# Optimization experiments

Hardware: AMD Instinct MI355X
Metric: run time of the kernel (lower is better)

Reference implementation:

```python
import jax, jax.numpy as jnp
import numpy as np

B, N, K = 4, 8192, 32
HID, INP = 64, 64
IN_CH = HID + INP  # 128; SetConv fc1 sees IN_CH + 3 (relative pos)


def setup_inputs() -> dict:
    key = jax.random.key(0)
    ks = jax.random.split(key, 10)
    return {
        "h": jax.random.normal(ks[0], (B, N, HID), jnp.float32),
        "x": jax.random.normal(ks[1], (B, N, INP), jnp.float32),
        "c": jax.random.normal(ks[2], (B, N, 3), jnp.float32),
        "W1": jax.random.normal(ks[3], (3, IN_CH + 3, HID), jnp.float32) * 0.05,
        "b1": jnp.zeros((3, HID), jnp.float32),
        "W2": jax.random.normal(ks[4], (3, HID, HID), jnp.float32) * 0.05,
        "b2": jnp.zeros((3, HID), jnp.float32),
        "W3": jax.random.normal(ks[5], (3, HID, HID), jnp.float32) * 0.05,
        "b3": jnp.zeros((3, HID), jnp.float32),
        "neigh_idx": jax.random.randint(ks[6], (B, N, K), 0, N, jnp.int32),
        "edge_feats": jax.random.normal(ks[7], (B, N, K, 3), jnp.float32),
    }


def reference(h, x, c, W1, b1, W2, b2, W3, b3, neigh_idx, edge_feats):
    # c (point coordinates) is unused by the GRU body, matching the torch source.
    slope = 0.1

    def setconv(i, feat):
        # gather K neighbor features per point: [B, N, K, C]
        g = jax.vmap(lambda fb, ib: fb[ib])(feat, neigh_idx)
        e = jnp.concatenate([g, edge_feats], axis=-1)  # [B, N, K, C+3]
        y = jax.nn.leaky_relu(jnp.einsum('bnkc,cd->bnkd', e, W1[i]) + b1[i], slope)
        y = y.max(axis=2)  # pool over neighbors -> [B, N, HID]
        y = jax.nn.leaky_relu(y @ W2[i] + b2[i], slope)
        return y @ W3[i] + b3[i]

    hx = jnp.concatenate([h, x], axis=2)
    z = jax.nn.sigmoid(setconv(0, hx))
    r = jax.nn.sigmoid(setconv(1, hx))
    q = jnp.tanh(setconv(2, jnp.concatenate([r * h, x], axis=2)))
    return (1.0 - z) * h + z * q
```

## Files before the change

### kernel.cpp

```cpp
#include <hip/hip_runtime.h>
#include <math.h>

typedef unsigned short u16;
typedef unsigned int u32;

#define KNBR 32

__device__ __forceinline__ float bf2f(u16 u) { return __uint_as_float((u32)u << 16); }
__device__ __forceinline__ float bflo(u32 u) { return __uint_as_float(u << 16); }
__device__ __forceinline__ float bfhi(u32 u) { return __uint_as_float(u & 0xffff0000u); }
__device__ __forceinline__ u16 f2bf(float f) {
    u32 u = __float_as_uint(f);
    return (u16)((u + 0x7fffu + ((u >> 16) & 1u)) >> 16);
}
__device__ __forceinline__ u32 pk2(float a, float b) {
    return (u32)f2bf(a) | ((u32)f2bf(b) << 16);
}
__device__ __forceinline__ float leaky(float v) { return v >= 0.f ? v : 0.1f * v; }
__device__ __forceinline__ float sigm(float v) { return 1.f / (1.f + expf(-v)); }

__device__ __forceinline__ int swz_plb(int b, int full) {
    if (!full) return b << 6;
    int xcd = b & 7;
    int within = ((b >> 3) << 1) | (xcd & 1);
    return ((xcd >> 1) << 13) + (within << 6);
}


__global__ __launch_bounds__(512) void k_gemm_p01(
    const float* __restrict__ h, const float* __restrict__ x,
    const float* __restrict__ W1f, const float* __restrict__ b1f,
    u32* __restrict__ P01, int p0, int full)
{
    __shared__ u32 a_lds[64 * 65];
    __shared__ float w_lds[2][64 * 64];
    int t = threadIdx.x;
    int plb = swz_plb(blockIdx.x, full);
    int pgb = p0 + plb;
    for (int i = 0; i < 8; ++i) {
        int id = t + i * 512;
        int p = id >> 6, cw = id & 63;
        const float* src = (cw < 32) ? (h + (size_t)(pgb + p) * 64 + cw * 2)
                                     : (x + (size_t)(pgb + p) * 64 + (cw - 32) * 2);
        float2 v = *(const float2*)src;
        a_lds[p * 65 + cw] = pk2(v.x, v.y);
    }
    int lane = t & 63;
    int cg = __builtin_amdgcn_readfirstlane(t >> 6);
    int di = lane & 15, pi = lane >> 4;
    int pt0 = cg * 8 + pi * 2;
    int dch = di * 4;
    float acc0[2][4], acc1[2][4];
    float4 bv0 = *(const float4*)&b1f[dch];
    float4 bv1 = *(const float4*)&b1f[64 + dch];
    #pragma unroll
    for (int pp = 0; pp < 2; ++pp) {
        acc0[pp][0] = bv0.x; acc0[pp][1] = bv0.y; acc0[pp][2] = bv0.z; acc0[pp][3] = bv0.w;
        acc1[pp][0] = bv1.x; acc1[pp][1] = bv1.y; acc1[pp][2] = bv1.z; acc1[pp][3] = bv1.w;
    }
    for (int half = 0; half < 2; ++half) {
        __syncthreads();
        for (int i = 0; i < 4; ++i) {
            int id = t + i * 512;
            int g = id >> 10, r = (id >> 4) & 63, d4 = id & 15;
            *(float4*)&w_lds[g][r * 64 + d4 * 4] =
                *(const float4*)(W1f + g * 8384 + (half * 64 + r) * 64 + d4 * 4);
        }
        __syncthreads();
        #pragma unroll 4
        for (int cw = 0; cw < 32; ++cw) {
            u32 aw0 = a_lds[(pt0 + 0) * 65 + half * 32 + cw];
            u32 aw1 = a_lds[(pt0 + 1) * 65 + half * 32 + cw];
            float4 wa0 = *(float4*)&w_lds[0][(2 * cw) * 64 + dch];
            float4 wa1 = *(float4*)&w_lds[0][(2 * cw + 1) * 64 + dch];
            float4 wb0 = *(float4*)&w_lds[1][(2 * cw) * 64 + dch];
            float4 wb1 = *(float4*)&w_lds[1][(2 * cw + 1) * 64 + dch];
            float a00 = bflo(aw0), a01 = bfhi(aw0);
            float a10 = bflo(aw1), a11 = bfhi(aw1);
            acc0[0][0] = fmaf(a00, wa0.x, acc0[0][0]); acc0[0][1] = fmaf(a00, wa0.y, acc0[0][1]);
            acc0[0][2] = fmaf(a00, wa0.z, acc0[0][2]); acc0[0][3] = fmaf(a00, wa0.w, acc0[0][3]);
            acc0[0][0] = fmaf(a01, wa1.x, acc0[0][0]); acc0[0][1] = fmaf(a01, wa1.y, acc0[0][1]);
            acc0[0][2] = fmaf(a01, wa1.z, acc0[0][2]); acc0[0][3] = fmaf(a01, wa1.w, acc0[0][3]);
            acc0[1][0] = fmaf(a10, wa0.x, acc0[1][0]); acc0[1][1] = fmaf(a10, wa0.y, acc0[1][1]);
            acc0[1][2] = fmaf(a10, wa0.z, acc0[1][2]); acc0[1][3] = fmaf(a10, wa0.w, acc0[1][3]);
            acc0[1][0] = fmaf(a11, wa1.x, acc0[1][0]); acc0[1][1] = fmaf(a11, wa1.y, acc0[1][1]);
            acc0[1][2] = fmaf(a11, wa1.z, acc0[1][2]); acc0[1][3] = fmaf(a11, wa1.w, acc0[1][3]);
            acc1[0][0] = fmaf(a00, wb0.x, acc1[0][0]); acc1[0][1] = fmaf(a00, wb0.y, acc1[0][1]);
            acc1[0][2] = fmaf(a00, wb0.z, acc1[0][2]); acc1[0][3] = fmaf(a00, wb0.w, acc1[0][3]);
            acc1[0][0] = fmaf(a01, wb1.x, acc1[0][0]); acc1[0][1] = fmaf(a01, wb1.y, acc1[0][1]);
            acc1[0][2] = fmaf(a01, wb1.z, acc1[0][2]); acc1[0][3] = fmaf(a01, wb1.w, acc1[0][3]);
            acc1[1][0] = fmaf(a10, wb0.x, acc1[1][0]); acc1[1][1] = fmaf(a10, wb0.y, acc1[1][1]);
            acc1[1][2] = fmaf(a10, wb0.z, acc1[1][2]); acc1[1][3] = fmaf(a10, wb0.w, acc1[1][3]);
            acc1[1][0] = fmaf(a11, wb1.x, acc1[1][0]); acc1[1][1] = fmaf(a11, wb1.y, acc1[1][1]);
            acc1[1][2] = fmaf(a11, wb1.z, acc1[1][2]); acc1[1][3] = fmaf(a11, wb1.w, acc1[1][3]);
        }
    }
    #pragma unroll
    for (int pp = 0; pp < 2; ++pp) {
        u32 o[4];
        #pragma unroll
        for (int j = 0; j < 4; ++j) o[j] = pk2(acc0[pp][j], acc1[pp][j]);
        *(uint4*)(P01 + (size_t)(plb + pt0 + pp) * 64 + dch) = *(uint4*)o;
    }
}

__global__ __launch_bounds__(512) void k_fuse01(
    const u32* __restrict__ P01, const float* __restrict__ W1f,
    const int* __restrict__ nidx, const float* __restrict__ ef,
    const float* __restrict__ h, const float* __restrict__ x,
    const float* __restrict__ W2f, const float* __restrict__ b2f,
    const float* __restrict__ W3f, const float* __restrict__ b3f,
    const float* __restrict__ b1f,
    u16* __restrict__ Z, u16* __restrict__ P2, int p0, int full)
{
    __shared__ u32 a_lds[64 * 65];
    __shared__ float w_lds[2][64 * 64];
    int t = threadIdx.x;
    int plb = swz_plb(blockIdx.x, full);
    int lane = t & 63;
    int cg = __builtin_amdgcn_readfirstlane(t >> 6);

    for (int i = 0; i < 4; ++i) {
        int id = t + i * 512;
        int g = id >> 10, r = (id >> 4) & 63, d4 = id & 15;
        *(float4*)&w_lds[g][r * 64 + d4 * 4] =
            *(const float4*)(W2f + g * 4096 + r * 64 + d4 * 4);
    }
    {
        u16* y16 = (u16*)a_lds;
        float w00 = W1f[8192 + lane], w01 = W1f[8256 + lane], w02 = W1f[8320 + lane];
        float w10 = W1f[16576 + lane], w11 = W1f[16640 + lane], w12 = W1f[16704 + lane];
        for (int pp = 0; pp < 8; ++pp) {
            int lp = cg * 8 + pp;
            int pg = p0 + plb + lp;
            int rbase = ((pg >> 13) << 13) - p0;
            const int* ni = nidx + (size_t)pg * KNBR;
            const float* ep = ef + (size_t)pg * KNBR * 3;
            float m0 = -1e30f, m1 = -1e30f;
            #pragma unroll 16
            for (int k = 0; k < KNBR; ++k) {
                int lr = rbase + ni[k];
                u32 g = P01[(size_t)lr * 64 + lane];
                float e0 = ep[3 * k], e1 = ep[3 * k + 1], e2 = ep[3 * k + 2];
                m0 = fmaxf(m0, bflo(g) + e0 * w00 + e1 * w01 + e2 * w02);
                m1 = fmaxf(m1, bfhi(g) + e0 * w10 + e1 * w11 + e2 * w12);
            }
            y16[lp * 130 + lane]      = f2bf(leaky(m0));
            y16[lp * 130 + 64 + lane] = f2bf(leaky(m1));
        }
    }
    __syncthreads();
    int g = cg >> 2, q = cg & 3;
    int di = lane & 15, pi = lane >> 4;
    int pt0 = q * 16 + pi * 4;
    int dch = di * 4;
    float acc[4][4];
    {
        float4 bv = *(const float4*)&b2f[g * 64 + dch];
        #pragma unroll
        for (int pp = 0; pp < 4; ++pp) {
            acc[pp][0] = bv.x; acc[pp][1] = bv.y; acc[pp][2] = bv.z; acc[pp][3] = bv.w;
        }
    }
    #pragma unroll 2
    for (int cw = 0; cw < 32; ++cw) {
        u32 aw[4];
        #pragma unroll
        for (int pp = 0; pp < 4; ++pp) aw[pp] = a_lds[(pt0 + pp) * 65 + g * 32 + cw];
        float4 w0 = *(float4*)&w_lds[g][(2 * cw) * 64 + dch];
        float4 w1 = *(float4*)&w_lds[g][(2 * cw + 1) * 64 + dch];
        #pragma unroll
        for (int pp = 0; pp < 4; ++pp) {
            float a0 = bflo(aw[pp]), a1 = bfhi(aw[pp]);
            acc[pp][0] = fmaf(a0, w0.x, acc[pp][0]);
            acc[pp][1] = fmaf(a0, w0.y, acc[pp][1]);
            acc[pp][2] = fmaf(a0, w0.z, acc[pp][2]);
            acc[pp][3] = fmaf(a0, w0.w, acc[pp][3]);
            acc[pp][0] = fmaf(a1, w1.x, acc[pp][0]);
            acc[pp][1] = fmaf(a1, w1.y, acc[pp][1]);
            acc[pp][2] = fmaf(a1, w1.z, acc[pp][2]);
            acc[pp][3] = fmaf(a1, w1.w, acc[pp][3]);
        }
    }
    __syncthreads();
    #pragma unroll
    for (int pp = 0; pp < 4; ++pp) {
        int base = (pt0 + pp) * 65 + g * 32 + di * 2;
        a_lds[base]     = pk2(leaky(acc[pp][0]), leaky(acc[pp][1]));
        a_lds[base + 1] = pk2(leaky(acc[pp][2]), leaky(acc[pp][3]));
    }
    for (int i = 0; i < 4; ++i) {
        int id = t + i * 512;
        int gg = id >> 10, r = (id >> 4) & 63, d4 = id & 15;
        *(float4*)&w_lds[gg][r * 64 + d4 * 4] =
            *(const float4*)(W3f + gg * 4096 + r * 64 + d4 * 4);
    }
    __syncthreads();
    {
        float4 bv = *(const float4*)&b3f[g * 64 + dch];
        #pragma unroll
        for (int pp = 0; pp < 4; ++pp) {
            acc[pp][0] = bv.x; acc[pp][1] = bv.y; acc[pp][2] = bv.z; acc[pp][3] = bv.w;
        }
    }
    #pragma unroll 2
    for (int cw = 0; cw < 32; ++cw) {
        u32 aw[4];
        #pragma unroll
        for (int pp = 0; pp < 4; ++pp) aw[pp] = a_lds[(pt0 + pp) * 65 + g * 32 + cw];
        float4 w0 = *(float4*)&w_lds[g][(2 * cw) * 64 + dch];
        float4 w1 = *(float4*)&w_lds[g][(2 * cw + 1) * 64 + dch];
        #pragma unroll
        for (int pp = 0; pp < 4; ++pp) {
            float a0 = bflo(aw[pp]), a1 = bfhi(aw[pp]);
            acc[pp][0] = fmaf(a0, w0.x, acc[pp][0]);
            acc[pp][1] = fmaf(a0, w0.y, acc[pp][1]);
            acc[pp][2] = fmaf(a0, w0.z, acc[pp][2]);
            acc[pp][3] = fmaf(a0, w0.w, acc[pp][3]);
            acc[pp][0] = fmaf(a1, w1.x, acc[pp][0]);
            acc[pp][1] = fmaf(a1, w1.y, acc[pp][1]);
            acc[pp][2] = fmaf(a1, w1.z, acc[pp][2]);
            acc[pp][3] = fmaf(a1, w1.w, acc[pp][3]);
        }
    }
    __syncthreads();
    if (g == 0) {
        #pragma unroll
        for (int pp = 0; pp < 4; ++pp) {
            int pl = plb + pt0 + pp;
            uint2 o;
            o.x = pk2(sigm(acc[pp][0]), sigm(acc[pp][1]));
            o.y = pk2(sigm(acc[pp][2]), sigm(acc[pp][3]));
            *(uint2*)(Z + (size_t)pl * 64 + dch) = o;
        }
    } else {
        #pragma unroll
        for (int pp = 0; pp < 4; ++pp) {
            int pg = p0 + plb + pt0 + pp;
            float4 hv = *(const float4*)&h[(size_t)pg * 64 + dch];
            int base = (pt0 + pp) * 65 + di * 2;
            a_lds[base]     = pk2(sigm(acc[pp][0]) * hv.x, sigm(acc[pp][1]) * hv.y);
            a_lds[base + 1] = pk2(sigm(acc[pp][2]) * hv.z, sigm(acc[pp][3]) * hv.w);
        }
    }
    for (int i = 0; i < 4; ++i) {
        int id = t + i * 512;
        int p = id >> 5, cw = id & 31;
        float2 v = *(const float2*)(x + (size_t)(p0 + plb + p) * 64 + cw * 2);
        a_lds[p * 65 + 32 + cw] = pk2(v.x, v.y);
    }
    float* wflat = (float*)w_lds;
    for (int i = 0; i < 4; ++i) {
        int id = t + i * 512;
        int r = id >> 4, d4 = id & 15;
        *(float4*)&wflat[r * 64 + d4 * 4] =
            *(const float4*)(W1f + 2 * 8384 + r * 64 + d4 * 4);
    }
    __syncthreads();
    int pt0b = cg * 8 + pi * 2;
    float pacc[2][4];
    {
        float4 bv = *(const float4*)&b1f[128 + dch];
        #pragma unroll
        for (int pp = 0; pp < 2; ++pp) {
            pacc[pp][0] = bv.x; pacc[pp][1] = bv.y; pacc[pp][2] = bv.z; pacc[pp][3] = bv.w;
        }
    }
    #pragma unroll 2
    for (int cw = 0; cw < 64; ++cw) {
        u32 aw0 = a_lds[(pt0b + 0) * 65 + cw];
        u32 aw1 = a_lds[(pt0b + 1) * 65 + cw];
        float4 w0 = *(float4*)&wflat[(2 * cw) * 64 + dch];
        float4 w1 = *(float4*)&wflat[(2 * cw + 1) * 64 + dch];
        float a00 = bflo(aw0), a01 = bfhi(aw0);
        float a10 = bflo(aw1), a11 = bfhi(aw1);
        pacc[0][0] = fmaf(a00, w0.x, pacc[0][0]); pacc[0][1] = fmaf(a00, w0.y, pacc[0][1]);
        pacc[0][2] = fmaf(a00, w0.z, pacc[0][2]); pacc[0][3] = fmaf(a00, w0.w, pacc[0][3]);
        pacc[0][0] = fmaf(a01, w1.x, pacc[0][0]); pacc[0][1] = fmaf(a01, w1.y, pacc[0][1]);
        pacc[0][2] = fmaf(a01, w1.z, pacc[0][2]); pacc[0][3] = fmaf(a01, w1.w, pacc[0][3]);
        pacc[1][0] = fmaf(a10, w0.x, pacc[1][0]); pacc[1][1] = fmaf(a10, w0.y, pacc[1][1]);
        pacc[1][2] = fmaf(a10, w0.z, pacc[1][2]); pacc[1][3] = fmaf(a10, w0.w, pacc[1][3]);
        pacc[1][0] = fmaf(a11, w1.x, pacc[1][0]); pacc[1][1] = fmaf(a11, w1.y, pacc[1][1]);
        pacc[1][2] = fmaf(a11, w1.z, pacc[1][2]); pacc[1][3] = fmaf(a11, w1.w, pacc[1][3]);
    }
    #pragma unroll
    for (int pp = 0; pp < 2; ++pp) {
        int pl = plb + pt0b + pp;
        uint2 o;
        o.x = pk2(pacc[pp][0], pacc[pp][1]);
        o.y = pk2(pacc[pp][2], pacc[pp][3]);
        *(uint2*)(P2 + (size_t)pl * 64 + dch) = o;
    }
}

__global__ __launch_bounds__(512) void k_fuse2(
    const u16* __restrict__ P2, const float* __restrict__ W1f,
    const int* __restrict__ nidx, const float* __restrict__ ef,
    const float* __restrict__ W2f, const float* __restrict__ b2f,
    const float* __restrict__ W3f, const float* __restrict__ b3f,
    const float* __restrict__ h, const u16* __restrict__ Z,
    float* __restrict__ out, int p0, int full)
{
    __shared__ u32 a_lds[64 * 33];
    __shared__ float w_lds[64 * 64];
    int t = threadIdx.x;
    int plb = swz_plb(blockIdx.x, full);
    int lane = t & 63;
    int cg = __builtin_amdgcn_readfirstlane(t >> 6);
    for (int i = 0; i < 2; ++i) {
        int id = t + i * 512;
        int r = (id >> 4) & 63, d4 = id & 15;
        *(float4*)&w_lds[r * 64 + d4 * 4] =
            *(const float4*)(W2f + 2 * 4096 + r * 64 + d4 * 4);
    }
    {
        const float* W = W1f + 2 * 8384;
        float w0 = W[8192 + lane], w1 = W[8256 + lane], w2 = W[8320 + lane];
        u16* y16 = (u16*)a_lds;
        for (int pp = 0; pp < 8; ++pp) {
            int lp = cg * 8 + pp;
            int pg = p0 + plb + lp;
            int rbase = ((pg >> 13) << 13) - p0;
            const int* ni = nidx + (size_t)pg * KNBR;
            const float* ep = ef + (size_t)pg * KNBR * 3;
            float m = -1e30f;
            #pragma unroll 16
            for (int k = 0; k < KNBR; ++k) {
                int lr = rbase + ni[k];
                float e0 = ep[3 * k], e1 = ep[3 * k + 1], e2 = ep[3 * k + 2];
                float v = bf2f(P2[(size_t)lr * 64 + lane]) + e0 * w0 + e1 * w1 + e2 * w2;
                m = fmaxf(m, v);
            }
            y16[lp * 66 + lane] = f2bf(leaky(m));
        }
    }
    __syncthreads();
    int di = lane & 15, pi = lane >> 4;
    int pt0 = cg * 8 + pi * 2;
    int dch = di * 4;
    float acc[2][4];
    {
        float4 bv = *(const float4*)&b2f[128 + dch];
        #pragma unroll
        for (int pp = 0; pp < 2; ++pp) {
            acc[pp][0] = bv.x; acc[pp][1] = bv.y; acc[pp][2] = bv.z; acc[pp][3] = bv.w;
        }
    }
    #pragma unroll 2
    for (int cw = 0; cw < 32; ++cw) {
        u32 aw0 = a_lds[(pt0 + 0) * 33 + cw];
        u32 aw1 = a_lds[(pt0 + 1) * 33 + cw];
        float4 w0 = *(float4*)&w_lds[(2 * cw) * 64 + dch];
        float4 w1 = *(float4*)&w_lds[(2 * cw + 1) * 64 + dch];
        float a00 = bflo(aw0), a01 = bfhi(aw0);
        float a10 = bflo(aw1), a11 = bfhi(aw1);
        acc[0][0] = fmaf(a00, w0.x, acc[0][0]); acc[0][1] = fmaf(a00, w0.y, acc[0][1]);
        acc[0][2] = fmaf(a00, w0.z, acc[0][2]); acc[0][3] = fmaf(a00, w0.w, acc[0][3]);
        acc[0][0] = fmaf(a01, w1.x, acc[0][0]); acc[0][1] = fmaf(a01, w1.y, acc[0][1]);
        acc[0][2] = fmaf(a01, w1.z, acc[0][2]); acc[0][3] = fmaf(a01, w1.w, acc[0][3]);
        acc[1][0] = fmaf(a10, w0.x, acc[1][0]); acc[1][1] = fmaf(a10, w0.y, acc[1][1]);
        acc[1][2] = fmaf(a10, w0.z, acc[1][2]); acc[1][3] = fmaf(a10, w0.w, acc[1][3]);
        acc[1][0] = fmaf(a11, w1.x, acc[1][0]); acc[1][1] = fmaf(a11, w1.y, acc[1][1]);
        acc[1][2] = fmaf(a11, w1.z, acc[1][2]); acc[1][3] = fmaf(a11, w1.w, acc[1][3]);
    }
    __syncthreads();
    #pragma unroll
    for (int pp = 0; pp < 2; ++pp) {
        int base = (pt0 + pp) * 33 + di * 2;
        a_lds[base]     = pk2(leaky(acc[pp][0]), leaky(acc[pp][1]));
        a_lds[base + 1] = pk2(leaky(acc[pp][2]), leaky(acc[pp][3]));
    }
    for (int i = 0; i < 2; ++i) {
        int id = t + i * 512;
        int r = (id >> 4) & 63, d4 = id & 15;
        *(float4*)&w_lds[r * 64 + d4 * 4] =
            *(const float4*)(W3f + 2 * 4096 + r * 64 + d4 * 4);
    }
    __syncthreads();
    {
        float4 bv = *(const float4*)&b3f[128 + dch];
        #pragma unroll
        for (int pp = 0; pp < 2; ++pp) {
            acc[pp][0] = bv.x; acc[pp][1] = bv.y; acc[pp][2] = bv.z; acc[pp][3] = bv.w;
        }
    }
    #pragma unroll 2
    for (int cw = 0; cw < 32; ++cw) {
        u32 aw0 = a_lds[(pt0 + 0) * 33 + cw];
        u32 aw1 = a_lds[(pt0 + 1) * 33 + cw];
        float4 w0 = *(float4*)&w_lds[(2 * cw) * 64 + dch];
        float4 w1 = *(float4*)&w_lds[(2 * cw + 1) * 64 + dch];
        float a00 = bflo(aw0), a01 = bfhi(aw0);
        float a10 = bflo(aw1), a11 = bfhi(aw1);
        acc[0][0] = fmaf(a00, w0.x, acc[0][0]); acc[0][1] = fmaf(a00, w0.y, acc[0][1]);
        acc[0][2] = fmaf(a00, w0.z, acc[0][2]); acc[0][3] = fmaf(a00, w0.w, acc[0][3]);
        acc[0][0] = fmaf(a01, w1.x, acc[0][0]); acc[0][1] = fmaf(a01, w1.y, acc[0][1]);
        acc[0][2] = fmaf(a01, w1.z, acc[0][2]); acc[0][3] = fmaf(a01, w1.w, acc[0][3]);
        acc[1][0] = fmaf(a10, w0.x, acc[1][0]); acc[1][1] = fmaf(a10, w0.y, acc[1][1]);
        acc[1][2] = fmaf(a10, w0.z, acc[1][2]); acc[1][3] = fmaf(a10, w0.w, acc[1][3]);
        acc[1][0] = fmaf(a11, w1.x, acc[1][0]); acc[1][1] = fmaf(a11, w1.y, acc[1][1]);
        acc[1][2] = fmaf(a11, w1.z, acc[1][2]); acc[1][3] = fmaf(a11, w1.w, acc[1][3]);
    }
    #pragma unroll
    for (int pp = 0; pp < 2; ++pp) {
        int pl = plb + pt0 + pp;
        int pg = p0 + pl;
        float4 hv = *(const float4*)&h[(size_t)pg * 64 + dch];
        uint2 zw = *(const uint2*)(Z + (size_t)pl * 64 + dch);
        float z0 = bflo(zw.x), z1 = bfhi(zw.x), z2 = bflo(zw.y), z3 = bfhi(zw.y);
        float4 o;
        o.x = (1.f - z0) * hv.x + z0 * tanhf(acc[pp][0]);
        o.y = (1.f - z1) * hv.y + z1 * tanhf(acc[pp][1]);
        o.z = (1.f - z2) * hv.z + z2 * tanhf(acc[pp][2]);
        o.w = (1.f - z3) * hv.w + z3 * tanhf(acc[pp][3]);
        *(float4*)&out[(size_t)pg * 64 + dch] = o;
    }
}

extern "C" void kernel_launch(void* const* d_in, const int* in_sizes, int n_in,
                              void* d_out, int out_size, void* d_ws, size_t ws_size,
                              hipStream_t stream)
{
    const float* h  = (const float*)d_in[0];
    const float* x  = (const float*)d_in[1];
    const float* W1 = (const float*)d_in[3];
    const float* b1 = (const float*)d_in[4];
    const float* W2 = (const float*)d_in[5];
    const float* b2 = (const float*)d_in[6];
    const float* W3 = (const float*)d_in[7];
    const float* b3 = (const float*)d_in[8];
    const int* nidx = (const int*)d_in[9];
    const float* ef = (const float*)d_in[10];
    float* out = (float*)d_out;

    char* wsb = (char*)d_ws;
    size_t PN = (ws_size >= 32768ull * 512ull) ? 32768 : 8192;
    int passes = (int)(32768 / PN);
    int full = (PN == 32768) ? 1 : 0;

    u32* P01 = (u32*)wsb;
    u16* Z   = (u16*)(wsb + PN * 256);
    u16* P2  = (u16*)(wsb + PN * 384);

    for (int s = 0; s < passes; ++s) {
        int p0 = (int)(s * PN);
        dim3 g((unsigned)(PN / 64));
        k_gemm_p01<<<g, 512, 0, stream>>>(h, x, W1, b1, P01, p0, full);
        k_fuse01  <<<g, 512, 0, stream>>>(P01, W1, nidx, ef, h, x,
                                          W2, b2, W3, b3, b1, Z, P2, p0, full);
        k_fuse2   <<<g, 512, 0, stream>>>(P2, W1, nidx, ef,
                                          W2, b2, W3, b3, h, Z, out, p0, full);
    }
}
```

Before: 199.9 us.

## Replace scalar FMA dense layers with bf16 MFMA across all three kernels

Rewrites the per-point dense matmuls (the fc1 projection, W2 and W3 layers) in all three kernels to use 16x16x32 bf16 MFMA instructions instead of scalar fp32 FMA loops. Weights are repacked in LDS as bf16 pairs in a transposed, padded layout that matches the MFMA operand shape. The P2 intermediate is also switched from bf16 to fp32, which raises the workspace requirement and changes the threshold for the single-pass path. The aim is to cut ALU-bound GEMM time. In exchange, the per-block weight repacking adds work, the output stores become scalar and less coalesced, and the larger fp32 P2 increases gather traffic.

```diff
diff --git a/kernel.cpp b/kernel.cpp
--- a/kernel.cpp
+++ b/kernel.cpp
@@ -3,8 +3,11 @@
 
 typedef unsigned short u16;
 typedef unsigned int u32;
+typedef __attribute__((ext_vector_type(8))) short s8v;
+typedef __attribute__((ext_vector_type(4))) float f4v;
 
 #define KNBR 32
+#define MFMA16(a, b, c) __builtin_amdgcn_mfma_f32_16x16x32_bf16((a), (b), (c), 0, 0, 0)
 
 __device__ __forceinline__ float bf2f(u16 u) { return __uint_as_float((u32)u << 16); }
 __device__ __forceinline__ float bflo(u32 u) { return __uint_as_float(u << 16); }
@@ -32,8 +35,8 @@
     const float* __restrict__ W1f, const float* __restrict__ b1f,
     u32* __restrict__ P01, int p0, int full)
 {
-    __shared__ u32 a_lds[64 * 65];
-    __shared__ float w_lds[2][64 * 64];
+    __shared__ u32 a_lds[64 * 68];
+    __shared__ u32 wb[2 * 64 * 68];
     int t = threadIdx.x;
     int plb = swz_plb(blockIdx.x, full);
     int pgb = p0 + plb;
@@ -43,65 +46,48 @@
         const float* src = (cw < 32) ? (h + (size_t)(pgb + p) * 64 + cw * 2)
                                      : (x + (size_t)(pgb + p) * 64 + (cw - 32) * 2);
         float2 v = *(const float2*)src;
-        a_lds[p * 65 + cw] = pk2(v.x, v.y);
-    }
+        a_lds[p * 68 + cw] = pk2(v.x, v.y);
+    }
+    for (int i = 0; i < 16; ++i) {
+        int id = t + i * 512;
+        int g = id >> 12, kp = (id >> 6) & 63, n = id & 63;
+        float w0 = W1f[g * 8384 + kp * 128 + n];
+        float w1 = W1f[g * 8384 + kp * 128 + 64 + n];
+        wb[(g * 64 + n) * 68 + kp] = pk2(w0, w1);
+    }
+    __syncthreads();
     int lane = t & 63;
-    int cg = __builtin_amdgcn_readfirstlane(t >> 6);
-    int di = lane & 15, pi = lane >> 4;
-    int pt0 = cg * 8 + pi * 2;
-    int dch = di * 4;
-    float acc0[2][4], acc1[2][4];
-    float4 bv0 = *(const float4*)&b1f[dch];
-    float4 bv1 = *(const float4*)&b1f[64 + dch];
-    #pragma unroll
-    for (int pp = 0; pp < 2; ++pp) {
-        acc0[pp][0] = bv0.x; acc0[pp][1] = bv0.y; acc0[pp][2] = bv0.z; acc0[pp][3] = bv0.w;
-        acc1[pp][0] = bv1.x; acc1[pp][1] = bv1.y; acc1[pp][2] = bv1.z; acc1[pp][3] = bv1.w;
-    }
-    for (int half = 0; half < 2; ++half) {
-        __syncthreads();
-        for (int i = 0; i < 4; ++i) {
-            int id = t + i * 512;
-            int g = id >> 10, r = (id >> 4) & 63, d4 = id & 15;
-            *(float4*)&w_lds[g][r * 64 + d4 * 4] =
-                *(const float4*)(W1f + g * 8384 + (half * 64 + r) * 64 + d4 * 4);
-        }
-        __syncthreads();
-        #pragma unroll 4
-        for (int cw = 0; cw < 32; ++cw) {
-            u32 aw0 = a_lds[(pt0 + 0) * 65 + half * 32 + cw];
-            u32 aw1 = a_lds[(pt0 + 1) * 65 + half * 32 + cw];
-            float4 wa0 = *(float4*)&w_lds[0][(2 * cw) * 64 + dch];
-            float4 wa1 = *(float4*)&w_lds[0][(2 * cw + 1) * 64 + dch];
-            float4 wb0 = *(float4*)&w_lds[1][(2 * cw) * 64 + dch];
-            float4 wb1 = *(float4*)&w_lds[1][(2 * cw + 1) * 64 + dch];
-            float a00 = bflo(aw0), a01 = bfhi(aw0);
-            float a10 = bflo(aw1), a11 = bfhi(aw1);
-            acc0[0][0] = fmaf(a00, wa0.x, acc0[0][0]); acc0[0][1] = fmaf(a00, wa0.y, acc0[0][1]);
-            acc0[0][2] = fmaf(a00, wa0.z, acc0[0][2]); acc0[0][3] = fmaf(a00, wa0.w, acc0[0][3]);
-            acc0[0][0] = fmaf(a01, wa1.x, acc0[0][0]); acc0[0][1] = fmaf(a01, wa1.y, acc0[0][1]);
-            acc0[0][2] = fmaf(a01, wa1.z, acc0[0][2]); acc0[0][3] = fmaf(a01, wa1.w, acc0[0][3]);
-            acc0[1][0] = fmaf(a10, wa0.x, acc0[1][0]); acc0[1][1] = fmaf(a10, wa0.y, acc0[1][1]);
-            acc0[1][2] = fmaf(a10, wa0.z, acc0[1][2]); acc0[1][3] = fmaf(a10, wa0.w, acc0[1][3]);
-            acc0[1][0] = fmaf(a11, wa1.x, acc0[1][0]); acc0[1][1] = fmaf(a11, wa1.y, acc0[1][1]);
-            acc0[1][2] = fmaf(a11, wa1.z, acc0[1][2]); acc0[1][3] = fmaf(a11, wa1.w, acc0[1][3]);
-            acc1[0][0] = fmaf(a00, wb0.x, acc1[0][0]); acc1[0][1] = fmaf(a00, wb0.y, acc1[0][1]);
-            acc1[0][2] = fmaf(a00, wb0.z, acc1[0][2]); acc1[0][3] = fmaf(a00, wb0.w, acc1[0][3]);
-            acc1[0][0] = fmaf(a01, wb1.x, acc1[0][0]); acc1[0][1] = fmaf(a01, wb1.y, acc1[0][1]);
-            acc1[0][2] = fmaf(a01, wb1.z, acc1[0][2]); acc1[0][3] = fmaf(a01, wb1.w, acc1[0][3]);
-            acc1[1][0] = fmaf(a10, wb0.x, acc1[1][0]); acc1[1][1] = fmaf(a10, wb0.y, acc1[1][1]);
-            acc1[1][2] = fmaf(a10, wb0.z, acc1[1][2]); acc1[1][3] = fmaf(a10, wb0.w, acc1[1][3]);
-            acc1[1][0] = fmaf(a11, wb1.x, acc1[1][0]); acc1[1][1] = fmaf(a11, wb1.y, acc1[1][1]);
-            acc1[1][2] = fmaf(a11, wb1.z, acc1[1][2]); acc1[1][3] = fmaf(a11, wb1.w, acc1[1][3]);
-        }
-    }
-    #pragma unroll
-    for (int pp = 0; pp < 2; ++pp) {
-        u32 o[4];
-        #pragma unroll
-        for (int j = 0; j < 4; ++j) o[j] = pk2(acc0[pp][j], acc1[pp][j]);
-        *(uint4*)(P01 + (size_t)(plb + pt0 + pp) * 64 + dch) = *(uint4*)o;
-    }
+    int w = __builtin_amdgcn_readfirstlane(t >> 6);
+    int m = w & 3, npair = w >> 2;
+    int quad = lane >> 4, l15 = lane & 15;
+    f4v acc[2][2];
+    #pragma unroll
+    for (int g = 0; g < 2; ++g)
+        #pragma unroll
+        for (int nt = 0; nt < 2; ++nt) {
+            float b = b1f[g * 64 + (npair * 2 + nt) * 16 + l15];
+            acc[g][nt] = (f4v){b, b, b, b};
+        }
+    #pragma unroll
+    for (int kb = 0; kb < 4; ++kb) {
+        s8v af = *(const s8v*)&a_lds[(m * 16 + l15) * 68 + kb * 16 + quad * 4];
+        #pragma unroll
+        for (int g = 0; g < 2; ++g)
+            #pragma unroll
+            for (int nt = 0; nt < 2; ++nt) {
+                s8v bf = *(const s8v*)&wb[(g * 64 + (npair * 2 + nt) * 16 + l15) * 68
+                                          + kb * 16 + quad * 4];
+                acc[g][nt] = MFMA16(af, bf, acc[g][nt]);
+            }
+    }
+    #pragma unroll
+    for (int nt = 0; nt < 2; ++nt)
+        #pragma unroll
+        for (int r = 0; r < 4; ++r) {
+            int pt = m * 16 + quad * 4 + r;
+            int ch = (npair * 2 + nt) * 16 + l15;
+            P01[(size_t)(plb + pt) * 64 + ch] = pk2(acc[0][nt][r], acc[1][nt][r]);
+        }
 }
 
 __global__ __launch_bounds__(512) void k_fuse01(
@@ -111,27 +97,29 @@
     const float* __restrict__ W2f, const float* __restrict__ b2f,
     const float* __restrict__ W3f, const float* __restrict__ b3f,
     const float* __restrict__ b1f,
-    u16* __restrict__ Z, u16* __restrict__ P2, int p0, int full)
+    u16* __restrict__ Z, float* __restrict__ P2, int p0, int full)
 {
-    __shared__ u32 a_lds[64 * 65];
-    __shared__ float w_lds[2][64 * 64];
+    __shared__ u32 a_lds[64 * 68];
+    __shared__ u32 wb[4608];
     int t = threadIdx.x;
     int plb = swz_plb(blockIdx.x, full);
     int lane = t & 63;
-    int cg = __builtin_amdgcn_readfirstlane(t >> 6);
-
-    for (int i = 0; i < 4; ++i) {
-        int id = t + i * 512;
-        int g = id >> 10, r = (id >> 4) & 63, d4 = id & 15;
-        *(float4*)&w_lds[g][r * 64 + d4 * 4] =
-            *(const float4*)(W2f + g * 4096 + r * 64 + d4 * 4);
+    int w = __builtin_amdgcn_readfirstlane(t >> 6);
+    int quad = lane >> 4, l15 = lane & 15;
+    u16* y16 = (u16*)a_lds;
+
+    for (int i = 0; i < 8; ++i) {
+        int id = t + i * 512;
+        int g = id >> 11, kp = (id >> 6) & 31, n = id & 63;
+        float w0 = W2f[g * 4096 + kp * 128 + n];
+        float w1 = W2f[g * 4096 + kp * 128 + 64 + n];
+        wb[(g * 64 + n) * 36 + kp] = pk2(w0, w1);
     }
     {
-        u16* y16 = (u16*)a_lds;
         float w00 = W1f[8192 + lane], w01 = W1f[8256 + lane], w02 = W1f[8320 + lane];
         float w10 = W1f[16576 + lane], w11 = W1f[16640 + lane], w12 = W1f[16704 + lane];
         for (int pp = 0; pp < 8; ++pp) {
-            int lp = cg * 8 + pp;
+            int lp = w * 8 + pp;
             int pg = p0 + plb + lp;
             int rbase = ((pg >> 13) << 13) - p0;
             const int* ni = nidx + (size_t)pg * KNBR;
@@ -140,185 +128,151 @@
             #pragma unroll 16
             for (int k = 0; k < KNBR; ++k) {
                 int lr = rbase + ni[k];
-                u32 g = P01[(size_t)lr * 64 + lane];
+                u32 gv = P01[(size_t)lr * 64 + lane];
                 float e0 = ep[3 * k], e1 = ep[3 * k + 1], e2 = ep[3 * k + 2];
-                m0 = fmaxf(m0, bflo(g) + e0 * w00 + e1 * w01 + e2 * w02);
-                m1 = fmaxf(m1, bfhi(g) + e0 * w10 + e1 * w11 + e2 * w12);
-            }
-            y16[lp * 130 + lane]      = f2bf(leaky(m0));
-            y16[lp * 130 + 64 + lane] = f2bf(leaky(m1));
-        }
-    }
-    __syncthreads();
-    int g = cg >> 2, q = cg & 3;
-    int di = lane & 15, pi = lane >> 4;
-    int pt0 = q * 16 + pi * 4;
-    int dch = di * 4;
-    float acc[4][4];
-    {
-        float4 bv = *(const float4*)&b2f[g * 64 + dch];
-        #pragma unroll
-        for (int pp = 0; pp < 4; ++pp) {
-            acc[pp][0] = bv.x; acc[pp][1] = bv.y; acc[pp][2] = bv.z; acc[pp][3] = bv.w;
-        }
-    }
-    #pragma unroll 2
-    for (int cw = 0; cw < 32; ++cw) {
-        u32 aw[4];
-        #pragma unroll
-        for (int pp = 0; pp < 4; ++pp) aw[pp] = a_lds[(pt0 + pp) * 65 + g * 32 + cw];
-        float4 w0 = *(float4*)&w_lds[g][(2 * cw) * 64 + dch];
-        float4 w1 = *(float4*)&w_lds[g][(2 * cw + 1) * 64 + dch];
-        #pragma unroll
-        for (int pp = 0; pp < 4; ++pp) {
-            float a0 = bflo(aw[pp]), a1 = bfhi(aw[pp]);
-            acc[pp][0] = fmaf(a0, w0.x, acc[pp][0]);
-            acc[pp][1] = fmaf(a0, w0.y, acc[pp][1]);
-            acc[pp][2] = fmaf(a0, w0.z, acc[pp][2]);
-            acc[pp][3] = fmaf(a0, w0.w, acc[pp][3]);
-            acc[pp][0] = fmaf(a1, w1.x, acc[pp][0]);
-            acc[pp][1] = fmaf(a1, w1.y, acc[pp][1]);
-            acc[pp][2] = fmaf(a1, w1.z, acc[pp][2]);
-            acc[pp][3] = fmaf(a1, w1.w, acc[pp][3]);
-        }
-    }
-    __syncthreads();
-    #pragma unroll
-    for (int pp = 0; pp < 4; ++pp) {
-        int base = (pt0 + pp) * 65 + g * 32 + di * 2;
-        a_lds[base]     = pk2(leaky(acc[pp][0]), leaky(acc[pp][1]));
-        a_lds[base + 1] = pk2(leaky(acc[pp][2]), leaky(acc[pp][3]));
-    }
-    for (int i = 0; i < 4; ++i) {
-        int id = t + i * 512;
-        int gg = id >> 10, r = (id >> 4) & 63, d4 = id & 15;
-        *(float4*)&w_lds[gg][r * 64 + d4 * 4] =
-            *(const float4*)(W3f + gg * 4096 + r * 64 + d4 * 4);
-    }
-    __syncthreads();
-    {
-        float4 bv = *(const float4*)&b3f[g * 64 + dch];
-        #pragma unroll
-        for (int pp = 0; pp < 4; ++pp) {
-            acc[pp][0] = bv.x; acc[pp][1] = bv.y; acc[pp][2] = bv.z; acc[pp][3] = bv.w;
-        }
-    }
-    #pragma unroll 2
-    for (int cw = 0; cw < 32; ++cw) {
-        u32 aw[4];
-        #pragma unroll
-        for (int pp = 0; pp < 4; ++pp) aw[pp] = a_lds[(pt0 + pp) * 65 + g * 32 + cw];
-        float4 w0 = *(float4*)&w_lds[g][(2 * cw) * 64 + dch];
-        float4 w1 = *(float4*)&w_lds[g][(2 * cw + 1) * 64 + dch];
-        #pragma unroll
-        for (int pp = 0; pp < 4; ++pp) {
-            float a0 = bflo(aw[pp]), a1 = bfhi(aw[pp]);
-            acc[pp][0] = fmaf(a0, w0.x, acc[pp][0]);
-            acc[pp][1] = fmaf(a0, w0.y, acc[pp][1]);
-            acc[pp][2] = fmaf(a0, w0.z, acc[pp][2]);
-            acc[pp][3] = fmaf(a0, w0.w, acc[pp][3]);
-            acc[pp][0] = fmaf(a1, w1.x, acc[pp][0]);
-            acc[pp][1] = fmaf(a1, w1.y, acc[pp][1]);
-            acc[pp][2] = fmaf(a1, w1.z, acc[pp][2]);
-            acc[pp][3] = fmaf(a1, w1.w, acc[pp][3]);
+                m0 = fmaxf(m0, bflo(gv) + e0 * w00 + e1 * w01 + e2 * w02);
+                m1 = fmaxf(m1, bfhi(gv) + e0 * w10 + e1 * w11 + e2 * w12);
+            }
+            y16[lp * 136 + lane]      = f2bf(leaky(m0));
+            y16[lp * 136 + 64 + lane] = f2bf(leaky(m1));
+        }
+    }
+    __syncthreads();
+    int m = w & 3, g = w >> 2;
+    f4v acc[4];
+    #pragma unroll
+    for (int nt = 0; nt < 4; ++nt) {
+        float b = b2f[g * 64 + nt * 16 + l15];
+        acc[nt] = (f4v){b, b, b, b};
+    }
+    #pragma unroll
+    for (int kb = 0; kb < 2; ++kb) {
+        s8v af = *(const s8v*)&a_lds[(m * 16 + l15) * 68 + g * 32 + kb * 16 + quad * 4];
+        #pragma unroll
+        for (int nt = 0; nt < 4; ++nt) {
+            s8v bf = *(const s8v*)&wb[(g * 64 + nt * 16 + l15) * 36 + kb * 16 + quad * 4];
+            acc[nt] = MFMA16(af, bf, acc[nt]);
+        }
+    }
+    #pragma unroll
+    for (int nt = 0; nt < 4; ++nt)
+        #pragma unroll
+        for (int r = 0; r < 4; ++r)
+            y16[(m * 16 + quad * 4 + r) * 136 + g * 64 + nt * 16 + l15] =
+                f2bf(leaky(acc[nt][r]));
+    __syncthreads();
+    for (int i = 0; i < 8; ++i) {
+        int id = t + i * 512;
+        int gg = id >> 11, kp = (id >> 6) & 31, n = id & 63;
+        float w0 = W3f[gg * 4096 + kp * 128 + n];
+        float w1 = W3f[gg * 4096 + kp * 128 + 64 + n];
+        wb[(gg * 64 + n) * 36 + kp] = pk2(w0, w1);
+    }
+    __syncthreads();
+    #pragma unroll
+    for (int nt = 0; nt < 4; ++nt) {
+        float b = b3f[g * 64 + nt * 16 + l15];
+        acc[nt] = (f4v){b, b, b, b};
+    }
+    #pragma unroll
+    for (int kb = 0; kb < 2; ++kb) {
+        s8v af = *(const s8v*)&a_lds[(m * 16 + l15) * 68 + g * 32 + kb * 16 + quad * 4];
+        #pragma unroll
+        for (int nt = 0; nt < 4; ++nt) {
+            s8v bf = *(const s8v*)&wb[(g * 64 + nt * 16 + l15) * 36 + kb * 16 + quad * 4];
+            acc[nt] = MFMA16(af, bf, acc[nt]);
         }
     }
     __syncthreads();
     if (g == 0) {
         #pragma unroll
-        for (int pp = 0; pp < 4; ++pp) {
-            int pl = plb + pt0 + pp;
-            uint2 o;
-            o.x = pk2(sigm(acc[pp][0]), sigm(acc[pp][1]));
-            o.y = pk2(sigm(acc[pp][2]), sigm(acc[pp][3]));
-            *(uint2*)(Z + (size_t)pl * 64 + dch) = o;
-        }
+        for (int nt = 0; nt < 4; ++nt)
+            #pragma unroll
+            for (int r = 0; r < 4; ++r) {
+                int pt = m * 16 + quad * 4 + r;
+                int ch = nt * 16 + l15;
+                Z[(size_t)(plb + pt) * 64 + ch] = f2bf(sigm(acc[nt][r]));
+            }
     } else {
         #pragma unroll
-        for (int pp = 0; pp < 4; ++pp) {
-            int pg = p0 + plb + pt0 + pp;
-            float4 hv = *(const float4*)&h[(size_t)pg * 64 + dch];
-            int base = (pt0 + pp) * 65 + di * 2;
-            a_lds[base]     = pk2(sigm(acc[pp][0]) * hv.x, sigm(acc[pp][1]) * hv.y);
-            a_lds[base + 1] = pk2(sigm(acc[pp][2]) * hv.z, sigm(acc[pp][3]) * hv.w);
-        }
+        for (int nt = 0; nt < 4; ++nt)
+            #pragma unroll
+            for (int r = 0; r < 4; ++r) {
+                int pt = m * 16 + quad * 4 + r;
+                int ch = nt * 16 + l15;
+                float hv = h[(size_t)(p0 + plb + pt) * 64 + ch];
+                y16[pt * 136 + ch] = f2bf(sigm(acc[nt][r]) * hv);
+            }
     }
     for (int i = 0; i < 4; ++i) {
         int id = t + i * 512;
         int p = id >> 5, cw = id & 31;
         float2 v = *(const float2*)(x + (size_t)(p0 + plb + p) * 64 + cw * 2);
-        a_lds[p * 65 + 32 + cw] = pk2(v.x, v.y);
-    }
-    float* wflat = (float*)w_lds;
-    for (int i = 0; i < 4; ++i) {
-        int id = t + i * 512;
-        int r = id >> 4, d4 = id & 15;
-        *(float4*)&wflat[r * 64 + d4 * 4] =
-            *(const float4*)(W1f + 2 * 8384 + r * 64 + d4 * 4);
-    }
-    __syncthreads();
-    int pt0b = cg * 8 + pi * 2;
-    float pacc[2][4];
-    {
-        float4 bv = *(const float4*)&b1f[128 + dch];
-        #pragma unroll
-        for (int pp = 0; pp < 2; ++pp) {
-            pacc[pp][0] = bv.x; pacc[pp][1] = bv.y; pacc[pp][2] = bv.z; pacc[pp][3] = bv.w;
-        }
-    }
-    #pragma unroll 2
-    for (int cw = 0; cw < 64; ++cw) {
-        u32 aw0 = a_lds[(pt0b + 0) * 65 + cw];
-        u32 aw1 = a_lds[(pt0b + 1) * 65 + cw];
-        float4 w0 = *(float4*)&wflat[(2 * cw) * 64 + dch];
-        float4 w1 = *(float4*)&wflat[(2 * cw + 1) * 64 + dch];
-        float a00 = bflo(aw0), a01 = bfhi(aw0);
-        float a10 = bflo(aw1), a11 = bfhi(aw1);
-        pacc[0][0] = fmaf(a00, w0.x, pacc[0][0]); pacc[0][1] = fmaf(a00, w0.y, pacc[0][1]);
-        pacc[0][2] = fmaf(a00, w0.z, pacc[0][2]); pacc[0][3] = fmaf(a00, w0.w, pacc[0][3]);
-        pacc[0][0] = fmaf(a01, w1.x, pacc[0][0]); pacc[0][1] = fmaf(a01, w1.y, pacc[0][1]);
-        pacc[0][2] = fmaf(a01, w1.z, pacc[0][2]); pacc[0][3] = fmaf(a01, w1.w, pacc[0][3]);
-        pacc[1][0] = fmaf(a10, w0.x, pacc[1][0]); pacc[1][1] = fmaf(a10, w0.y, pacc[1][1]);
-        pacc[1][2] = fmaf(a10, w0.z, pacc[1][2]); pacc[1][3] = fmaf(a10, w0.w, pacc[1][3]);
-        pacc[1][0] = fmaf(a11, w1.x, pacc[1][0]); pacc[1][1] = fmaf(a11, w1.y, pacc[1][1]);
-        pacc[1][2] = fmaf(a11, w1.z, pacc[1][2]); pacc[1][3] = fmaf(a11, w1.w, pacc[1][3]);
-    }
-    #pragma unroll
-    for (int pp = 0; pp < 2; ++pp) {
-        int pl = plb + pt0b + pp;
-        uint2 o;
-        o.x = pk2(pacc[pp][0], pacc[pp][1]);
-        o.y = pk2(pacc[pp][2], pacc[pp][3]);
-        *(uint2*)(P2 + (size_t)pl * 64 + dch) = o;
-    }
+        a_lds[p * 68 + 32 + cw] = pk2(v.x, v.y);
+    }
+    for (int i = 0; i < 8; ++i) {
+        int id = t + i * 512;
+        int kp = (id >> 6) & 63, n = id & 63;
+        float w0 = W1f[2 * 8384 + kp * 128 + n];
+        float w1 = W1f[2 * 8384 + kp * 128 + 64 + n];
+        wb[n * 68 + kp] = pk2(w0, w1);
+    }
+    __syncthreads();
+    int nh = w >> 2;
+    f4v pacc[2];
+    #pragma unroll
+    for (int nt = 0; nt < 2; ++nt) {
+        float b = b1f[128 + (nh * 2 + nt) * 16 + l15];
+        pacc[nt] = (f4v){b, b, b, b};
+    }
+    #pragma unroll
+    for (int kb = 0; kb < 4; ++kb) {
+        s8v af = *(const s8v*)&a_lds[(m * 16 + l15) * 68 + kb * 16 + quad * 4];
+        #pragma unroll
+        for (int nt = 0; nt < 2; ++nt) {
+            s8v bf = *(const s8v*)&wb[((nh * 2 + nt) * 16 + l15) * 68 + kb * 16 + quad * 4];
+            pacc[nt] = MFMA16(af, bf, pacc[nt]);
+        }
+    }
+    #pragma unroll
+    for (int nt = 0; nt < 2; ++nt)
+        #pragma unroll
+        for (int r = 0; r < 4; ++r) {
+            int pt = m * 16 + quad * 4 + r;
+            int ch = (nh * 2 + nt) * 16 + l15;
+            P2[(size_t)(plb + pt) * 64 + ch] = pacc[nt][r];
+        }
 }
 
 __global__ __launch_bounds__(512) void k_fuse2(
-    const u16* __restrict__ P2, const float* __restrict__ W1f,
+    const float* __restrict__ P2, const float* __restrict__ W1f,
     const int* __restrict__ nidx, const float* __restrict__ ef,
     const float* __restrict__ W2f, const float* __restrict__ b2f,
     const float* __restrict__ W3f, const float* __restrict__ b3f,
     const float* __restrict__ h, const u16* __restrict__ Z,
     float* __restrict__ out, int p0, int full)
 {
-    __shared__ u32 a_lds[64 * 33];
-    __shared__ float w_lds[64 * 64];
+    __shared__ u32 a_lds[64 * 36];
+    __shared__ u32 wb[64 * 36];
     int t = threadIdx.x;
     int plb = swz_plb(blockIdx.x, full);
     int lane = t & 63;
-    int cg = __builtin_amdgcn_readfirstlane(t >> 6);
-    for (int i = 0; i < 2; ++i) {
-        int id = t + i * 512;
-        int r = (id >> 4) & 63, d4 = id & 15;
-        *(float4*)&w_lds[r * 64 + d4 * 4] =
-            *(const float4*)(W2f + 2 * 4096 + r * 64 + d4 * 4);
+    int w = __builtin_amdgcn_readfirstlane(t >> 6);
+    int quad = lane >> 4, l15 = lane & 15;
+    u16* y16 = (u16*)a_lds;
+
+    for (int i = 0; i < 4; ++i) {
+        int id = t + i * 512;
+        int kp = (id >> 6) & 31, n = id & 63;
+        float w0 = W2f[2 * 4096 + kp * 128 + n];
+        float w1 = W2f[2 * 4096 + kp * 128 + 64 + n];
+        wb[n * 36 + kp] = pk2(w0, w1);
     }
     {
         const float* W = W1f + 2 * 8384;
         float w0 = W[8192 + lane], w1 = W[8256 + lane], w2 = W[8320 + lane];
-        u16* y16 = (u16*)a_lds;
         for (int pp = 0; pp < 8; ++pp) {
-            int lp = cg * 8 + pp;
+            int lp = w * 8 + pp;
             int pg = p0 + plb + lp;
             int rbase = ((pg >> 13) << 13) - p0;
             const int* ni = nidx + (size_t)pg * KNBR;
@@ -328,93 +282,70 @@
             for (int k = 0; k < KNBR; ++k) {
                 int lr = rbase + ni[k];
                 float e0 = ep[3 * k], e1 = ep[3 * k + 1], e2 = ep[3 * k + 2];
-                float v = bf2f(P2[(size_t)lr * 64 + lane]) + e0 * w0 + e1 * w1 + e2 * w2;
+                float v = P2[(size_t)lr * 64 + lane] + e0 * w0 + e1 * w1 + e2 * w2;
                 m = fmaxf(m, v);
             }
-            y16[lp * 66 + lane] = f2bf(leaky(m));
-        }
-    }
-    __syncthreads();
-    int di = lane & 15, pi = lane >> 4;
-    int pt0 = cg * 8 + pi * 2;
-    int dch = di * 4;
-    float acc[2][4];
-    {
-        float4 bv = *(const float4*)&b2f[128 + dch];
-        #pragma unroll
-        for (int pp = 0; pp < 2; ++pp) {
-            acc[pp][0] = bv.x; acc[pp][1] = bv.y; acc[pp][2] = bv.z; acc[pp][3] = bv.w;
-        }
-    }
-    #pragma unroll 2
-    for (int cw = 0; cw < 32; ++cw) {
-        u32 aw0 = a_lds[(pt0 + 0) * 33 + cw];
-        u32 aw1 = a_lds[(pt0 + 1) * 33 + cw];
-        float4 w0 = *(float4*)&w_lds[(2 * cw) * 64 + dch];
-        float4 w1 = *(float4*)&w_lds[(2 * cw + 1) * 64 + dch];
-        float a00 = bflo(aw0), a01 = bfhi(aw0);
-        float a10 = bflo(aw1), a11 = bfhi(aw1);
-        acc[0][0] = fmaf(a00, w0.x, acc[0][0]); acc[0][1] = fmaf(a00, w0.y, acc[0][1]);
-        acc[0][2] = fmaf(a00, w0.z, acc[0][2]); acc[0][3] = fmaf(a00, w0.w, acc[0][3]);
-        acc[0][0] = fmaf(a01, w1.x, acc[0][0]); acc[0][1] = fmaf(a01, w1.y, acc[0][1]);
-        acc[0][2] = fmaf(a01, w1.z, acc[0][2]); acc[0][3] = fmaf(a01, w1.w, acc[0][3]);
-        acc[1][0] = fmaf(a10, w0.x, acc[1][0]); acc[1][1] = fmaf(a10, w0.y, acc[1][1]);
-        acc[1][2] = fmaf(a10, w0.z, acc[1][2]); acc[1][3] = fmaf(a10, w0.w, acc[1][3]);
-        acc[1][0] = fmaf(a11, w1.x, acc[1][0]); acc[1][1] = fmaf(a11, w1.y, acc[1][1]);
-        acc[1][2] = fmaf(a11, w1.z, acc[1][2]); acc[1][3] = fmaf(a11, w1.w, acc[1][3]);
-    }
-    __syncthreads();
-    #pragma unroll
-    for (int pp = 0; pp < 2; ++pp) {
-        int base = (pt0 + pp) * 33 + di * 2;
-        a_lds[base]     = pk2(leaky(acc[pp][0]), leaky(acc[pp][1]));
-        a_lds[base + 1] = pk2(leaky(acc[pp][2]), leaky(acc[pp][3]));
-    }
-    for (int i = 0; i < 2; ++i) {
-        int id = t + i * 512;
-        int r = (id >> 4) & 63, d4 = id & 15;
-        *(float4*)&w_lds[r * 64 + d4 * 4] =
-            *(const float4*)(W3f + 2 * 4096 + r * 64 + d4 * 4);
-    }
-    __syncthreads();
-    {
-        float4 bv = *(const float4*)&b3f[128 + dch];
-        #pragma unroll
-        for (int pp = 0; pp < 2; ++pp) {
-            acc[pp][0] = bv.x; acc[pp][1] = bv.y; acc[pp][2] = bv.z; acc[pp][3] = bv.w;
-        }
-    }
-    #pragma unroll 2
-    for (int cw = 0; cw < 32; ++cw) {
-        u32 aw0 = a_lds[(pt0 + 0) * 33 + cw];
-        u32 aw1 = a_lds[(pt0 + 1) * 33 + cw];
-        float4 w0 = *(float4*)&w_lds[(2 * cw) * 64 + dch];
-        float4 w1 = *(float4*)&w_lds[(2 * cw + 1) * 64 + dch];
-        float a00 = bflo(aw0), a01 = bfhi(aw0);
-        float a10 = bflo(aw1), a11 = bfhi(aw1);
-        acc[0][0] = fmaf(a00, w0.x, acc[0][0]); acc[0][1] = fmaf(a00, w0.y, acc[0][1]);
-        acc[0][2] = fmaf(a00, w0.z, acc[0][2]); acc[0][3] = fmaf(a00, w0.w, acc[0][3]);
-        acc[0][0] = fmaf(a01, w1.x, acc[0][0]); acc[0][1] = fmaf(a01, w1.y, acc[0][1]);
-        acc[0][2] = fmaf(a01, w1.z, acc[0][2]); acc[0][3] = fmaf(a01, w1.w, acc[0][3]);
-        acc[1][0] = fmaf(a10, w0.x, acc[1][0]); acc[1][1] = fmaf(a10, w0.y, acc[1][1]);
-        acc[1][2] = fmaf(a10, w0.z, acc[1][2]); acc[1][3] = fmaf(a10, w0.w, acc[1][3]);
-        acc[1][0] = fmaf(a11, w1.x, acc[1][0]); acc[1][1] = fmaf(a11, w1.y, acc[1][1]);
-        acc[1][2] = fmaf(a11, w1.z, acc[1][2]); acc[1][3] = fmaf(a11, w1.w, acc[1][3]);
-    }
-    #pragma unroll
-    for (int pp = 0; pp < 2; ++pp) {
-        int pl = plb + pt0 + pp;
-        int pg = p0 + pl;
-        float4 hv = *(const float4*)&h[(size_t)pg * 64 + dch];
-        uint2 zw = *(const uint2*)(Z + (size_t)pl * 64 + dch);
-        float z0 = bflo(zw.x), z1 = bfhi(zw.x), z2 = bflo(zw.y), z3 = bfhi(zw.y);
-        float4 o;
-        o.x = (1.f - z0) * hv.x + z0 * tanhf(acc[pp][0]);
-        o.y = (1.f - z1) * hv.y + z1 * tanhf(acc[pp][1]);
-        o.z = (1.f - z2) * hv.z + z2 * tanhf(acc[pp][2]);
-        o.w = (1.f - z3) * hv.w + z3 * tanhf(acc[pp][3]);
-        *(float4*)&out[(size_t)pg * 64 + dch] = o;
-    }
+            y16[lp * 72 + lane] = f2bf(leaky(m));
+        }
+    }
+    __syncthreads();
+    int m = w & 3, nh = w >> 2;
+    f4v acc[2];
+    #pragma unroll
+    for (int nt = 0; nt < 2; ++nt) {
+        float b = b2f[128 + (nh * 2 + nt) * 16 + l15];
+        acc[nt] = (f4v){b, b, b, b};
+    }
+    #pragma unroll
+    for (int kb = 0; kb < 2; ++kb) {
+        s8v af = *(const s8v*)&a_lds[(m * 16 + l15) * 36 + kb * 16 + quad * 4];
+        #pragma unroll
+        for (int nt = 0; nt < 2; ++nt) {
+            s8v bf = *(const s8v*)&wb[((nh * 2 + nt) * 16 + l15) * 36 + kb * 16 + quad * 4];
+            acc[nt] = MFMA16(af, bf, acc[nt]);
+        }
+    }
+    __syncthreads();
+    #pragma unroll
+    for (int nt = 0; nt < 2; ++nt)
+        #pragma unroll
+        for (int r = 0; r < 4; ++r)
+            y16[(m * 16 + quad * 4 + r) * 72 + (nh * 2 + nt) * 16 + l15] =
+                f2bf(leaky(acc[nt][r]));
+    for (int i = 0; i < 4; ++i) {
+        int id = t + i * 512;
+        int kp = (id >> 6) & 31, n = id & 63;
+        float w0 = W3f[2 * 4096 + kp * 128 + n];
+        float w1 = W3f[2 * 4096 + kp * 128 + 64 + n];
+        wb[n * 36 + kp] = pk2(w0, w1);
+    }
+    __syncthreads();
+    #pragma unroll
+    for (int nt = 0; nt < 2; ++nt) {
+        float b = b3f[128 + (nh * 2 + nt) * 16 + l15];
+        acc[nt] = (f4v){b, b, b, b};
+    }
+    #pragma unroll
+    for (int kb = 0; kb < 2; ++kb) {
+        s8v af = *(const s8v*)&a_lds[(m * 16 + l15) * 36 + kb * 16 + quad * 4];
+        #pragma unroll
+        for (int nt = 0; nt < 2; ++nt) {
+            s8v bf = *(const s8v*)&wb[((nh * 2 + nt) * 16 + l15) * 36 + kb * 16 + quad * 4];
+            acc[nt] = MFMA16(af, bf, acc[nt]);
+        }
+    }
+    #pragma unroll
+    for (int nt = 0; nt < 2; ++nt)
+        #pragma unroll
+        for (int r = 0; r < 4; ++r) {
+            int pt = m * 16 + quad * 4 + r;
+            int ch = (nh * 2 + nt) * 16 + l15;
+            int pl = plb + pt;
+            int pg = p0 + pl;
+            float z = bf2f(Z[(size_t)pl * 64 + ch]);
+            float hv = h[(size_t)pg * 64 + ch];
+            out[(size_t)pg * 64 + ch] = (1.f - z) * hv + z * tanhf(acc[nt][r]);
+        }
 }
 
 extern "C" void kernel_launch(void* const* d_in, const int* in_sizes, int n_in,
@@ -434,13 +365,13 @@
     float* out = (float*)d_out;
 
     char* wsb = (char*)d_ws;
-    size_t PN = (ws_size >= 32768ull * 512ull) ? 32768 : 8192;
+    size_t PN = (ws_size >= 32768ull * 640ull) ? 32768 : 8192;
     int passes = (int)(32768 / PN);
     int full = (PN == 32768) ? 1 : 0;
 
-    u32* P01 = (u32*)wsb;
-    u16* Z   = (u16*)(wsb + PN * 256);
-    u16* P2  = (u16*)(wsb + PN * 384);
+    u32* P01  = (u32*)wsb;
+    u16* Z    = (u16*)(wsb + PN * 256);
+    float* P2 = (float*)(wsb + PN * 384);
 
     for (int s = 0; s < passes; ++s) {
         int p0 = (int)(s * PN);
```

Result: faster. 182.8 us (-8.6%).
